# Kernel optimization log

Measured on AMD Instinct MI355X. Metric: run time of the kernel, lower is better.

Reference implementation:

```python
import jax, jax.numpy as jnp
import numpy as np

N, E, D_IN, L, H, U = 20000, 320000, 256, 4, 4, 64
HID = H * U  # 256
OUT = 64
LN_EPS = 1e-3  # keras LayerNormalization default epsilon
NEG_SLOPE = 0.2


def layer_norm(x, g, b):
    m = jnp.mean(x, axis=-1, keepdims=True)
    v = jnp.var(x, axis=-1, keepdims=True)
    return (x - m) * jax.lax.rsqrt(v + LN_EPS) * g + b


def gatv2(x, dst, src, Wl, Wr, a):
    # x: [N, HID]; Wl/Wr: [HID, H, U]; a: [H, U]
    zl = jnp.einsum('nd,dhu->nhu', x, Wl)  # target projection
    zr = jnp.einsum('nd,dhu->nhu', x, Wr)  # source projection / messages
    f = jax.nn.leaky_relu(zl[dst] + zr[src], NEG_SLOPE)       # [E, H, U]
    s = jnp.einsum('ehu,hu->eh', f, a)                        # [E, H]
    smax = jax.ops.segment_max(s, dst, num_segments=N)        # [N, H]
    es = jnp.exp(s - smax[dst])
    denom = jax.ops.segment_sum(es, dst, num_segments=N)      # [N, H]
    agg = jax.ops.segment_sum(es[:, :, None] * zr[src], dst, num_segments=N)
    agg = agg / (denom[:, :, None] + 1e-9)                    # [N, H, U]
    return agg.reshape(N, HID) + x  # residual (input dim == H*U)


def setup_inputs() -> dict:
    key = jax.random.key(0)
    ks = jax.random.split(key, 10)
    s_in = 1.0 / np.sqrt(D_IN)
    s_h = 1.0 / np.sqrt(HID)
    return {
        'x': jax.random.normal(ks[0], (N, D_IN), jnp.float32),
        'head_W': jax.random.normal(ks[1], (D_IN, HID), jnp.float32) * s_in,
        'head_b': jnp.zeros((HID,), jnp.float32),
        'ng_g': jnp.ones((L, HID), jnp.float32),
        'ng_b': jnp.zeros((L, HID), jnp.float32),
        'Wl': jax.random.normal(ks[2], (L, HID, H, U), jnp.float32) * s_h,
        'Wr': jax.random.normal(ks[3], (L, HID, H, U), jnp.float32) * s_h,
        'att': jax.random.normal(ks[4], (L, H, U), jnp.float32) * (1.0 / np.sqrt(U)),
        'nd_g': jnp.ones((L, HID), jnp.float32),
        'nd_b': jnp.zeros((L, HID), jnp.float32),
        'dense_W': jax.random.normal(ks[5], (L, HID, 4 * HID), jnp.float32) * s_h,
        'dense_b': jnp.zeros((L, 4 * HID), jnp.float32),
        'tail_W': jax.random.normal(ks[6], (HID, OUT), jnp.float32) * s_h,
        'tail_b': jnp.zeros((OUT,), jnp.float32),
        'edges': jax.random.randint(ks[7], (E, 2), 0, N, jnp.int32),
    }


def reference(x, head_W, head_b, ng_g, ng_b, Wl, Wr, att, nd_g, nd_b,
              dense_W, dense_b, tail_W, tail_b, edges):
    dst, src = edges[:, 0], edges[:, 1]
    h = x @ head_W + head_b  # head_layer
    for l in range(L):
        h = layer_norm(h, ng_g[l], ng_b[l])
        h = gatv2(h, dst, src, Wl[l], Wr[l], att[l])
        xr = layer_norm(h, nd_g[l], nd_b[l])
        # inference: dropout is identity
        d = jax.nn.gelu(xr @ dense_W[l] + dense_b[l], approximate=True)  # [N, 4*HID]
        h = d.reshape(N, 4, HID).sum(axis=1) + xr  # Add(split(.,4)) + residual
    return h @ tail_W + tail_b
```

## Files before the change

### kernel.cpp

```cpp
#include <hip/hip_runtime.h>
#include <cstdint>

#define NN 20000
#define EE 320000
#define DHID 256

typedef short bf16x8 __attribute__((ext_vector_type(8)));
typedef float f32x4 __attribute__((ext_vector_type(4)));


__device__ __forceinline__ float b2f(unsigned short u) {
    union { unsigned int i; float f; } v;
    v.i = ((unsigned int)u) << 16;
    return v.f;
}

__device__ __forceinline__ void b2f2(unsigned int w, float& lo, float& hi) {
    union { unsigned int i; float f; } a, c;
    a.i = w << 16;
    c.i = w & 0xffff0000u;
    lo = a.f;
    hi = c.f;
}

__device__ __forceinline__ unsigned short f2b(float x) {
    union { float f; unsigned int i; } v;
    v.f = x;
    unsigned int r = (v.i + 0x7FFFu + ((v.i >> 16) & 1u)) >> 16;
    return (unsigned short)r;
}

__device__ __forceinline__ float wave_sum(float v) {
#pragma unroll
    for (int m = 1; m < 64; m <<= 1) v += __shfl_xor(v, m);
    return v;
}

__device__ __forceinline__ float quad16_sum(float v) {
#pragma unroll
    for (int m = 1; m < 16; m <<= 1) v += __shfl_xor(v, m);
    return v;
}

__device__ __forceinline__ float gelu_f(float x) {
    float z = 0.7978845608028654f * (x + 0.044715f * x * x * x);
    float e = __expf(2.0f * z);
    float t = 1.0f - 2.0f / (e + 1.0f);
    return 0.5f * x * (1.0f + t);
}

__device__ __forceinline__ void gld16(const unsigned short* g, unsigned short* lds) {
    __builtin_amdgcn_global_load_lds((const __attribute__((address_space(1))) unsigned int*)g,
                                     (__attribute__((address_space(3))) unsigned int*)lds, 16, 0, 0);
}


__global__ void hist_kernel(const int* __restrict__ edges, int* __restrict__ counts, int E_) {
    int e = blockIdx.x * 256 + threadIdx.x;
    if (e >= E_) return;
    atomicAdd(&counts[edges[e * 2]], 1);
}

__global__ __launch_bounds__(1024) void scan_block(const int* __restrict__ counts,
                                                   int* __restrict__ excl,
                                                   int* __restrict__ bsums, int n) {
    __shared__ int sd[1024];
    int tid = threadIdx.x;
    int i = blockIdx.x * 1024 + tid;
    int c = (i < n) ? counts[i] : 0;
    sd[tid] = c;
    __syncthreads();
#pragma unroll
    for (int off = 1; off < 1024; off <<= 1) {
        int v = (tid >= off) ? sd[tid - off] : 0;
        __syncthreads();
        sd[tid] += v;
        __syncthreads();
    }
    if (i < n) excl[i] = sd[tid] - c;
    if (tid == 1023) bsums[blockIdx.x] = sd[1023];
}

__global__ void scan_tops(int* __restrict__ bsums, int nb) {
    if (threadIdx.x == 0 && blockIdx.x == 0) {
        int run = 0;
        for (int i = 0; i < nb; ++i) { int t = bsums[i]; bsums[i] = run; run += t; }
    }
}

__global__ void scan_fix(const int* __restrict__ excl, const int* __restrict__ bsums,
                         int* __restrict__ indptr, int* __restrict__ cursor, int n) {
    int i = blockIdx.x * 256 + threadIdx.x;
    if (i < n) {
        int v = excl[i] + bsums[i >> 10];
        indptr[i] = v;
        cursor[i] = v;
    }
    if (i == 0) indptr[n] = EE;
}

__global__ void scatter_kernel(const int* __restrict__ edges, int* __restrict__ cursor,
                               int* __restrict__ ssrc, int E_) {
    int e = blockIdx.x * 256 + threadIdx.x;
    if (e >= E_) return;
    int dstn = edges[e * 2];
    int src  = edges[e * 2 + 1];
    int pos = atomicAdd(&cursor[dstn], 1);
    ssrc[pos] = src;
}


__global__ __launch_bounds__(256) void transpose_bf16(const float* __restrict__ W,
                                                      unsigned short* __restrict__ Wt,
                                                      int K, int M, size_t lsW, size_t lsT) {
    W  += (size_t)blockIdx.z * lsW;
    Wt += (size_t)blockIdx.z * lsT;
    __shared__ float sm[32][33];
    int m0 = blockIdx.x * 32, k0 = blockIdx.y * 32;
    int tx = threadIdx.x & 31, ty = threadIdx.x >> 5;
#pragma unroll
    for (int i = 0; i < 4; ++i)
        sm[ty + i * 8][tx] = W[(size_t)(k0 + ty + i * 8) * M + m0 + tx];
    __syncthreads();
#pragma unroll
    for (int i = 0; i < 4; ++i)
        Wt[(size_t)(m0 + ty + i * 8) * K + k0 + tx] = f2b(sm[tx][ty + i * 8]);
}

__global__ void convert_bf16(const float* __restrict__ in, unsigned short* __restrict__ out, int n4) {
    int i = blockIdx.x * 256 + threadIdx.x;
    if (i >= n4) return;
    float4 v = *(const float4*)(in + (size_t)i * 4);
    ushort4 o;
    o.x = f2b(v.x); o.y = f2b(v.y); o.z = f2b(v.z); o.w = f2b(v.w);
    *(ushort4*)(out + (size_t)i * 4) = o;
}


__global__ __launch_bounds__(256) void ln_kernel(const float* __restrict__ X,
                                                 const float* __restrict__ g,
                                                 const float* __restrict__ b,
                                                 float* __restrict__ Y,
                                                 unsigned short* __restrict__ Yb, int nrows) {
    int row = blockIdx.x * 4 + (threadIdx.x >> 6);
    int lane = threadIdx.x & 63;
    if (row >= nrows) return;
    float4 v = *(const float4*)(X + (size_t)row * DHID + lane * 4);
    float sum = wave_sum(v.x + v.y + v.z + v.w);
    float sq  = wave_sum(v.x * v.x + v.y * v.y + v.z * v.z + v.w * v.w);
    float mean = sum * (1.0f / DHID);
    float var  = sq * (1.0f / DHID) - mean * mean;
    float r = rsqrtf(fmaxf(var, 0.0f) + 1e-3f);
    float4 gv = *(const float4*)(g + lane * 4);
    float4 bv = *(const float4*)(b + lane * 4);
    float4 o;
    o.x = (v.x - mean) * r * gv.x + bv.x;
    o.y = (v.y - mean) * r * gv.y + bv.y;
    o.z = (v.z - mean) * r * gv.z + bv.z;
    o.w = (v.w - mean) * r * gv.w + bv.w;
    *(float4*)(Y + (size_t)row * DHID + lane * 4) = o;
    ushort4 ob;
    ob.x = f2b(o.x); ob.y = f2b(o.y); ob.z = f2b(o.z); ob.w = f2b(o.w);
    *(ushort4*)(Yb + (size_t)row * DHID + lane * 4) = ob;
}

__global__ __launch_bounds__(256) void ln_dense(const unsigned short* __restrict__ d,
                                                const float* __restrict__ xr,
                                                const float* __restrict__ g,
                                                const float* __restrict__ b,
                                                float* __restrict__ Y,
                                                unsigned short* __restrict__ Yb, int nrows) {
    int row = blockIdx.x * 4 + (threadIdx.x >> 6);
    int lane = threadIdx.x & 63;
    if (row >= nrows) return;
    float4 v = *(const float4*)(xr + (size_t)row * DHID + lane * 4);
#pragma unroll
    for (int c = 0; c < 4; ++c) {
        ushort4 t = *(const ushort4*)(d + (size_t)row * 1024 + c * 256 + lane * 4);
        v.x += b2f(t.x); v.y += b2f(t.y); v.z += b2f(t.z); v.w += b2f(t.w);
    }
    float sum = wave_sum(v.x + v.y + v.z + v.w);
    float sq  = wave_sum(v.x * v.x + v.y * v.y + v.z * v.z + v.w * v.w);
    float mean = sum * (1.0f / DHID);
    float var  = sq * (1.0f / DHID) - mean * mean;
    float r = rsqrtf(fmaxf(var, 0.0f) + 1e-3f);
    float4 gv = *(const float4*)(g + lane * 4);
    float4 bv = *(const float4*)(b + lane * 4);
    float4 o;
    o.x = (v.x - mean) * r * gv.x + bv.x;
    o.y = (v.y - mean) * r * gv.y + bv.y;
    o.z = (v.z - mean) * r * gv.z + bv.z;
    o.w = (v.w - mean) * r * gv.w + bv.w;
    *(float4*)(Y + (size_t)row * DHID + lane * 4) = o;
    ushort4 ob;
    ob.x = f2b(o.x); ob.y = f2b(o.y); ob.z = f2b(o.z); ob.w = f2b(o.w);
    *(ushort4*)(Yb + (size_t)row * DHID + lane * 4) = ob;
}

__global__ __launch_bounds__(256) void combine_final(const unsigned short* __restrict__ d,
                                                     const float* __restrict__ xr,
                                                     unsigned short* __restrict__ hb, int nrows) {
    int row = blockIdx.x * 4 + (threadIdx.x >> 6);
    int lane = threadIdx.x & 63;
    if (row >= nrows) return;
    float4 v = *(const float4*)(xr + (size_t)row * DHID + lane * 4);
#pragma unroll
    for (int c = 0; c < 4; ++c) {
        ushort4 t = *(const ushort4*)(d + (size_t)row * 1024 + c * 256 + lane * 4);
        v.x += b2f(t.x); v.y += b2f(t.y); v.z += b2f(t.z); v.w += b2f(t.w);
    }
    ushort4 ob;
    ob.x = f2b(v.x); ob.y = f2b(v.y); ob.z = f2b(v.z); ob.w = f2b(v.w);
    *(ushort4*)(hb + (size_t)row * DHID + lane * 4) = ob;
}


#define CS_STRIDE 140

template <int EP>
__global__ __launch_bounds__(256, 3) void gemm128(const unsigned short* __restrict__ A,
                                                  const unsigned short* __restrict__ B,
                                                  const float* __restrict__ bias,
                                                  void* __restrict__ Cv, int nrows, int ncols) {
    __shared__ unsigned short As[128 * 32];
    __shared__ unsigned short Bs[128 * 32];
    __shared__ unsigned short Cs[128 * CS_STRIDE];
    const int bm = blockIdx.x * 128, bn = blockIdx.y * 128;
    if (bm >= nrows) return;
    const int tid  = threadIdx.x;
    const int w    = tid >> 6, lane = tid & 63;
    const int quad = lane >> 4, l16 = lane & 15;
    const int wm = w >> 1, wn = w & 1;

    const int srow = lane & 15;
    const int sg   = lane >> 4;
    int ga0 = min(bm + w * 32 + srow,      nrows - 1);
    int ga1 = min(bm + w * 32 + 16 + srow, nrows - 1);
    int gb0 = min(bn + w * 32 + srow,      ncols - 1);
    int gb1 = min(bn + w * 32 + 16 + srow, ncols - 1);
    const unsigned short* Ap0 = A + (size_t)ga0 * 256 + sg * 8;
    const unsigned short* Ap1 = A + (size_t)ga1 * 256 + sg * 8;
    const unsigned short* Bp0 = B + (size_t)gb0 * 256 + sg * 8;
    const unsigned short* Bp1 = B + (size_t)gb1 * 256 + sg * 8;
    unsigned short* la0 = As + (2 * w) * 512;
    unsigned short* la1 = As + (2 * w + 1) * 512;
    unsigned short* lb0 = Bs + (2 * w) * 512;
    unsigned short* lb1 = Bs + (2 * w + 1) * 512;

    f32x4 acc[4][4] = {};
    for (int k0 = 0; k0 < 256; k0 += 32) {
        gld16(Ap0 + k0, la0);
        gld16(Ap1 + k0, la1);
        gld16(Bp0 + k0, lb0);
        gld16(Bp1 + k0, lb1);
        __syncthreads();
        bf16x8 a[4], b[4];
#pragma unroll
        for (int mi = 0; mi < 4; ++mi)
            a[mi] = *(const bf16x8*)(As + (wm * 4 + mi) * 512 + quad * 128 + l16 * 8);
#pragma unroll
        for (int ni = 0; ni < 4; ++ni)
            b[ni] = *(const bf16x8*)(Bs + (wn * 4 + ni) * 512 + quad * 128 + l16 * 8);
#pragma unroll
        for (int mi = 0; mi < 4; ++mi)
#pragma unroll
            for (int ni = 0; ni < 4; ++ni)
                acc[mi][ni] = __builtin_amdgcn_mfma_f32_16x16x32_bf16(a[mi], b[ni], acc[mi][ni], 0, 0, 0);
        __syncthreads();
    }

    if (EP == 0) {
#pragma unroll
        for (int ni = 0; ni < 4; ++ni) {
            int col = bn + wn * 64 + ni * 16 + l16;
            if (col >= ncols) continue;
            float bv = bias ? bias[col] : 0.0f;
#pragma unroll
            for (int mi = 0; mi < 4; ++mi) {
#pragma unroll
                for (int r = 0; r < 4; ++r) {
                    int row = bm + wm * 64 + mi * 16 + quad * 4 + r;
                    if (row < nrows) ((float*)Cv)[(size_t)row * ncols + col] = acc[mi][ni][r] + bv;
                }
            }
        }
    } else {
#pragma unroll
        for (int ni = 0; ni < 4; ++ni) {
            int lc = wn * 64 + ni * 16 + l16;
            float bv = (EP == 2) ? bias[bn + lc] : 0.0f;
#pragma unroll
            for (int mi = 0; mi < 4; ++mi) {
#pragma unroll
                for (int r = 0; r < 4; ++r) {
                    int lr = wm * 64 + mi * 16 + quad * 4 + r;
                    float v = acc[mi][ni][r] + bv;
                    Cs[lr * CS_STRIDE + lc] = f2b(EP == 2 ? gelu_f(v) : v);
                }
            }
        }
        __syncthreads();
#pragma unroll
        for (int i = 0; i < 8; ++i) {
            int id = tid + 256 * i;
            int lr = id >> 4;
            int lc = (id & 15) * 8;
            int grow = bm + lr;
            if (grow < nrows) {
                uint4 val = *(const uint4*)(Cs + lr * CS_STRIDE + lc);
                *(uint4*)((unsigned short*)Cv + (size_t)grow * ncols + bn + lc) = val;
            }
        }
    }
}


__global__ __launch_bounds__(256) void gat_fused(const unsigned short* __restrict__ zb,
                                                 const float* __restrict__ att,
                                                 const int* __restrict__ ssrc,
                                                 const int* __restrict__ indptr,
                                                 const float* __restrict__ hn,
                                                 const float* __restrict__ g,
                                                 const float* __restrict__ b,
                                                 float* __restrict__ xr,
                                                 unsigned short* __restrict__ xrb, int nrows) {
    int wid = threadIdx.x >> 6;
    int lane = threadIdx.x & 63;
    int n = blockIdx.x * 4 + wid;
    if (n >= nrows) return;
    int start = indptr[n];
    int end = indptr[n + 1];

    ushort4 zlu = *(const ushort4*)(zb + (size_t)n * 512 + lane * 4);
    float zl0 = b2f(zlu.x), zl1 = b2f(zlu.y), zl2 = b2f(zlu.z), zl3 = b2f(zlu.w);
    float4 a4 = *(const float4*)(att + lane * 4);
    size_t idx = (size_t)n * DHID + lane * 4;
    float4 rres = *(const float4*)(hn + idx);

    float m = -3.0e38f, denom = 0.f;
    float ax = 0.f, ay = 0.f, az = 0.f, aw = 0.f;

    const uint2* zrp = (const uint2*)(zb + 256);
    uint2 c0 = make_uint2(0, 0), c1 = make_uint2(0, 0);
    if (start < end) {
        int i0 = ssrc[start];
        int i1 = ssrc[(start + 1 < end) ? start + 1 : start];
        c0 = zrp[(size_t)i0 * 128 + lane];
        c1 = zrp[(size_t)i1 * 128 + lane];
    }
    for (int p = start; p < end; p += 2) {
        uint2 u0 = c0, u1 = c1;
        bool val1 = (p + 1 < end);
        if (p + 2 < end) {
            int j0 = ssrc[p + 2];
            int j1 = ssrc[(p + 3 < end) ? p + 3 : p + 2];
            c0 = zrp[(size_t)j0 * 128 + lane];
            c1 = zrp[(size_t)j1 * 128 + lane];
        }
        float z00, z01, z02, z03, z10, z11, z12, z13;
        b2f2(u0.x, z00, z01); b2f2(u0.y, z02, z03);
        b2f2(u1.x, z10, z11); b2f2(u1.y, z12, z13);

        float v0 = zl0 + z00, v1 = zl1 + z01, v2 = zl2 + z02, v3 = zl3 + z03;
        float t0 = zl0 + z10, t1 = zl1 + z11, t2 = zl2 + z12, t3 = zl3 + z13;
        v0 = (v0 > 0.f) ? v0 : 0.2f * v0;
        v1 = (v1 > 0.f) ? v1 : 0.2f * v1;
        v2 = (v2 > 0.f) ? v2 : 0.2f * v2;
        v3 = (v3 > 0.f) ? v3 : 0.2f * v3;
        t0 = (t0 > 0.f) ? t0 : 0.2f * t0;
        t1 = (t1 > 0.f) ? t1 : 0.2f * t1;
        t2 = (t2 > 0.f) ? t2 : 0.2f * t2;
        t3 = (t3 > 0.f) ? t3 : 0.2f * t3;
        float part0 = a4.x * v0 + a4.y * v1 + a4.z * v2 + a4.w * v3;
        float part1 = a4.x * t0 + a4.y * t1 + a4.z * t2 + a4.w * t3;
        float sp0 = quad16_sum(part0);
        float sp1 = quad16_sum(part1);
        if (!val1) sp1 = -3.0e38f;
        float newm = fmaxf(m, fmaxf(sp0, sp1));
        float corr = __expf(m - newm);
        float w0 = __expf(sp0 - newm);
        float w1 = __expf(sp1 - newm);
        denom = denom * corr + w0 + w1;
        ax = ax * corr + w0 * z00 + w1 * z10;
        ay = ay * corr + w0 * z01 + w1 * z11;
        az = az * corr + w0 * z02 + w1 * z12;
        aw = aw * corr + w0 * z03 + w1 * z13;
        m = newm;
    }
    float inv = 1.0f / (denom + 1e-9f);
    float4 o;
    o.x = ax * inv + rres.x;
    o.y = ay * inv + rres.y;
    o.z = az * inv + rres.z;
    o.w = aw * inv + rres.w;
    float sum = wave_sum(o.x + o.y + o.z + o.w);
    float sq  = wave_sum(o.x * o.x + o.y * o.y + o.z * o.z + o.w * o.w);
    float mean = sum * (1.0f / DHID);
    float var  = sq * (1.0f / DHID) - mean * mean;
    float rr = rsqrtf(fmaxf(var, 0.0f) + 1e-3f);
    float4 gv = *(const float4*)(g + lane * 4);
    float4 bv = *(const float4*)(b + lane * 4);
    float4 y;
    y.x = (o.x - mean) * rr * gv.x + bv.x;
    y.y = (o.y - mean) * rr * gv.y + bv.y;
    y.z = (o.z - mean) * rr * gv.z + bv.z;
    y.w = (o.w - mean) * rr * gv.w + bv.w;
    *(float4*)(xr + idx) = y;
    ushort4 ob;
    ob.x = f2b(y.x); ob.y = f2b(y.y); ob.z = f2b(y.z); ob.w = f2b(y.w);
    *(ushort4*)(xrb + idx) = ob;
}


extern "C" void kernel_launch(void* const* d_in, const int* in_sizes, int n_in,
                              void* d_out, int out_size, void* d_ws, size_t ws_size,
                              hipStream_t stream) {
    const float* x       = (const float*)d_in[0];
    const float* head_W  = (const float*)d_in[1];
    const float* head_b  = (const float*)d_in[2];
    const float* ng_g    = (const float*)d_in[3];
    const float* ng_b    = (const float*)d_in[4];
    const float* Wl      = (const float*)d_in[5];
    const float* Wr      = (const float*)d_in[6];
    const float* att     = (const float*)d_in[7];
    const float* nd_g    = (const float*)d_in[8];
    const float* nd_b    = (const float*)d_in[9];
    const float* dense_W = (const float*)d_in[10];
    const float* dense_b = (const float*)d_in[11];
    const float* tail_W  = (const float*)d_in[12];
    const float* tail_b  = (const float*)d_in[13];
    const int*   edges   = (const int*)d_in[14];
    float* out = (float*)d_out;

    const size_t NH = (size_t)NN * DHID;
    float* xr = (float*)d_ws;
    float* hn = xr + NH;
    unsigned short* hnb = (unsigned short*)(hn + NH);
    unsigned short* xrb = hnb + NH;
    unsigned short* U   = xrb + NH;
    unsigned short* zb  = U;
    unsigned short* d_buf = U;
    unsigned short* headT  = U + 4 * NH;
    unsigned short* WzT    = headT + 65536;
    unsigned short* denseT = WzT + 524288;
    unsigned short* tailT  = denseT + 1048576;
    int* counts = (int*)(tailT + 16384);
    int* bsums  = counts + NN;
    int* excl   = bsums + 32;
    int* indptr = excl + NN;
    int* cursor = indptr + NN + 1;
    int* ssrc   = cursor + NN;

    hipMemsetAsync(counts, 0, NN * sizeof(int), stream);
    hist_kernel<<<(EE + 255) / 256, 256, 0, stream>>>(edges, counts, EE);
    scan_block<<<(NN + 1023) / 1024, 1024, 0, stream>>>(counts, excl, bsums, NN);
    scan_tops<<<1, 64, 0, stream>>>(bsums, (NN + 1023) / 1024);
    scan_fix<<<(NN + 255) / 256, 256, 0, stream>>>(excl, bsums, indptr, cursor, NN);
    scatter_kernel<<<(EE + 255) / 256, 256, 0, stream>>>(edges, cursor, ssrc, EE);

    transpose_bf16<<<dim3(8, 8, 1), 256, 0, stream>>>(head_W, headT, 256, 256, 0, 0);
    transpose_bf16<<<dim3(8, 8, 4), 256, 0, stream>>>(Wl, WzT, 256, 256, 65536, 131072);
    transpose_bf16<<<dim3(8, 8, 4), 256, 0, stream>>>(Wr, WzT + 65536, 256, 256, 65536, 131072);
    transpose_bf16<<<dim3(32, 8, 4), 256, 0, stream>>>(dense_W, denseT, 256, 1024, 262144, 262144);
    transpose_bf16<<<dim3(2, 8, 1), 256, 0, stream>>>(tail_W, tailT, 256, 64, 0, 0);
    convert_bf16<<<(int)(NH / 4 + 255) / 256, 256, 0, stream>>>(x, hnb, (int)(NH / 4));

    const int GXP = 160;
    gemm128<0><<<dim3(GXP, 2), 256, 0, stream>>>(hnb, headT, head_b, xr, NN, 256);

    for (int l = 0; l < 4; ++l) {
        if (l == 0)
            ln_kernel<<<NN / 4, 256, 0, stream>>>(xr, ng_g, ng_b, hn, hnb, NN);
        else
            ln_dense<<<NN / 4, 256, 0, stream>>>(d_buf, xr, ng_g + l * 256, ng_b + l * 256, hn, hnb, NN);
        gemm128<1><<<dim3(GXP, 4), 256, 0, stream>>>(hnb, WzT + (size_t)l * 131072, nullptr, zb, NN, 512);
        gat_fused<<<(NN + 3) / 4, 256, 0, stream>>>(zb, att + l * 256, ssrc, indptr, hn,
                                                    nd_g + l * 256, nd_b + l * 256, xr, xrb, NN);
        gemm128<2><<<dim3(GXP, 8), 256, 0, stream>>>(xrb, denseT + (size_t)l * 262144,
                                                     dense_b + l * 1024, d_buf, NN, 1024);
    }
    combine_final<<<NN / 4, 256, 0, stream>>>(d_buf, xr, hnb, NN);
    gemm128<0><<<dim3(GXP, 1), 256, 0, stream>>>(hnb, tailT, tail_b, out, NN, 64);
}
```

Measured before the change: 644.8 us.

## Alias GEMM epilogue staging onto tile smem and unroll GAT edge loop by four

```diff
diff --git a/kernel.cpp b/kernel.cpp
--- a/kernel.cpp
+++ b/kernel.cpp
@@ -215,16 +215,17 @@
 }
 
 
-#define CS_STRIDE 140
+#define CS 132
 
 template <int EP>
-__global__ __launch_bounds__(256, 3) void gemm128(const unsigned short* __restrict__ A,
+__global__ __launch_bounds__(256, 5) void gemm128(const unsigned short* __restrict__ A,
                                                   const unsigned short* __restrict__ B,
                                                   const float* __restrict__ bias,
                                                   void* __restrict__ Cv, int nrows, int ncols) {
-    __shared__ unsigned short As[128 * 32];
-    __shared__ unsigned short Bs[128 * 32];
-    __shared__ unsigned short Cs[128 * CS_STRIDE];
+    __shared__ unsigned short smem[8448];
+    unsigned short* As = smem;
+    unsigned short* Bs = smem + 4096;
+    unsigned short* Cs = smem;
     const int bm = blockIdx.x * 128, bn = blockIdx.y * 128;
     if (bm >= nrows) return;
     const int tid  = threadIdx.x;
@@ -286,30 +287,36 @@
         }
     } else {
 #pragma unroll
-        for (int ni = 0; ni < 4; ++ni) {
-            int lc = wn * 64 + ni * 16 + l16;
-            float bv = (EP == 2) ? bias[bn + lc] : 0.0f;
-#pragma unroll
-            for (int mi = 0; mi < 4; ++mi) {
-#pragma unroll
-                for (int r = 0; r < 4; ++r) {
-                    int lr = wm * 64 + mi * 16 + quad * 4 + r;
-                    float v = acc[mi][ni][r] + bv;
-                    Cs[lr * CS_STRIDE + lc] = f2b(EP == 2 ? gelu_f(v) : v);
+        for (int half = 0; half < 2; ++half) {
+            if (wm == half) {
+#pragma unroll
+                for (int ni = 0; ni < 4; ++ni) {
+                    int lc = wn * 64 + ni * 16 + l16;
+                    float bv = (EP == 2) ? bias[bn + lc] : 0.0f;
+#pragma unroll
+                    for (int mi = 0; mi < 4; ++mi) {
+#pragma unroll
+                        for (int r = 0; r < 4; ++r) {
+                            int lr = mi * 16 + quad * 4 + r;
+                            float v = acc[mi][ni][r] + bv;
+                            Cs[lr * CS + lc] = f2b(EP == 2 ? gelu_f(v) : v);
+                        }
+                    }
                 }
             }
-        }
-        __syncthreads();
-#pragma unroll
-        for (int i = 0; i < 8; ++i) {
-            int id = tid + 256 * i;
-            int lr = id >> 4;
-            int lc = (id & 15) * 8;
-            int grow = bm + lr;
-            if (grow < nrows) {
-                uint4 val = *(const uint4*)(Cs + lr * CS_STRIDE + lc);
-                *(uint4*)((unsigned short*)Cv + (size_t)grow * ncols + bn + lc) = val;
+            __syncthreads();
+#pragma unroll
+            for (int i = 0; i < 4; ++i) {
+                int id = tid + 256 * i;
+                int lr = id >> 4;
+                int lc = (id & 15) * 8;
+                int grow = bm + half * 64 + lr;
+                if (grow < nrows) {
+                    uint4 val = *(const uint4*)(Cs + lr * CS + lc);
+                    *(uint4*)((unsigned short*)Cv + (size_t)grow * ncols + bn + lc) = val;
+                }
             }
+            __syncthreads();
         }
     }
 }
@@ -341,50 +348,55 @@
     float ax = 0.f, ay = 0.f, az = 0.f, aw = 0.f;
 
     const uint2* zrp = (const uint2*)(zb + 256);
-    uint2 c0 = make_uint2(0, 0), c1 = make_uint2(0, 0);
+    uint2 c[4];
+#pragma unroll
+    for (int j = 0; j < 4; ++j) c[j] = make_uint2(0, 0);
     if (start < end) {
-        int i0 = ssrc[start];
-        int i1 = ssrc[(start + 1 < end) ? start + 1 : start];
-        c0 = zrp[(size_t)i0 * 128 + lane];
-        c1 = zrp[(size_t)i1 * 128 + lane];
-    }
-    for (int p = start; p < end; p += 2) {
-        uint2 u0 = c0, u1 = c1;
-        bool val1 = (p + 1 < end);
-        if (p + 2 < end) {
-            int j0 = ssrc[p + 2];
-            int j1 = ssrc[(p + 3 < end) ? p + 3 : p + 2];
-            c0 = zrp[(size_t)j0 * 128 + lane];
-            c1 = zrp[(size_t)j1 * 128 + lane];
+#pragma unroll
+        for (int j = 0; j < 4; ++j) {
+            int q = min(start + j, end - 1);
+            c[j] = zrp[(size_t)ssrc[q] * 128 + lane];
         }
-        float z00, z01, z02, z03, z10, z11, z12, z13;
-        b2f2(u0.x, z00, z01); b2f2(u0.y, z02, z03);
-        b2f2(u1.x, z10, z11); b2f2(u1.y, z12, z13);
-
-        float v0 = zl0 + z00, v1 = zl1 + z01, v2 = zl2 + z02, v3 = zl3 + z03;
-        float t0 = zl0 + z10, t1 = zl1 + z11, t2 = zl2 + z12, t3 = zl3 + z13;
-        v0 = (v0 > 0.f) ? v0 : 0.2f * v0;
-        v1 = (v1 > 0.f) ? v1 : 0.2f * v1;
-        v2 = (v2 > 0.f) ? v2 : 0.2f * v2;
-        v3 = (v3 > 0.f) ? v3 : 0.2f * v3;
-        t0 = (t0 > 0.f) ? t0 : 0.2f * t0;
-        t1 = (t1 > 0.f) ? t1 : 0.2f * t1;
-        t2 = (t2 > 0.f) ? t2 : 0.2f * t2;
-        t3 = (t3 > 0.f) ? t3 : 0.2f * t3;
-        float part0 = a4.x * v0 + a4.y * v1 + a4.z * v2 + a4.w * v3;
-        float part1 = a4.x * t0 + a4.y * t1 + a4.z * t2 + a4.w * t3;
-        float sp0 = quad16_sum(part0);
-        float sp1 = quad16_sum(part1);
-        if (!val1) sp1 = -3.0e38f;
-        float newm = fmaxf(m, fmaxf(sp0, sp1));
+    }
+    for (int p = start; p < end; p += 4) {
+        uint2 u[4];
+#pragma unroll
+        for (int j = 0; j < 4; ++j) u[j] = c[j];
+        if (p + 4 < end) {
+#pragma unroll
+            for (int j = 0; j < 4; ++j) {
+                int q = min(p + 4 + j, end - 1);
+                c[j] = zrp[(size_t)ssrc[q] * 128 + lane];
+            }
+        }
+        float z[4][4], sp[4];
+#pragma unroll
+        for (int j = 0; j < 4; ++j) {
+            b2f2(u[j].x, z[j][0], z[j][1]);
+            b2f2(u[j].y, z[j][2], z[j][3]);
+            float v0 = zl0 + z[j][0], v1 = zl1 + z[j][1];
+            float v2 = zl2 + z[j][2], v3 = zl3 + z[j][3];
+            v0 = (v0 > 0.f) ? v0 : 0.2f * v0;
+            v1 = (v1 > 0.f) ? v1 : 0.2f * v1;
+            v2 = (v2 > 0.f) ? v2 : 0.2f * v2;
+            v3 = (v3 > 0.f) ? v3 : 0.2f * v3;
+            float part = a4.x * v0 + a4.y * v1 + a4.z * v2 + a4.w * v3;
+            sp[j] = quad16_sum(part);
+        }
+#pragma unroll
+        for (int j = 1; j < 4; ++j)
+            if (p + j >= end) sp[j] = -3.0e38f;
+        float newm = fmaxf(fmaxf(m, fmaxf(sp[0], sp[1])), fmaxf(sp[2], sp[3]));
         float corr = __expf(m - newm);
-        float w0 = __expf(sp0 - newm);
-        float w1 = __expf(sp1 - newm);
-        denom = denom * corr + w0 + w1;
-        ax = ax * corr + w0 * z00 + w1 * z10;
-        ay = ay * corr + w0 * z01 + w1 * z11;
-        az = az * corr + w0 * z02 + w1 * z12;
-        aw = aw * corr + w0 * z03 + w1 * z13;
+        float w0 = __expf(sp[0] - newm);
+        float w1 = __expf(sp[1] - newm);
+        float w2 = __expf(sp[2] - newm);
+        float w3 = __expf(sp[3] - newm);
+        denom = denom * corr + w0 + w1 + w2 + w3;
+        ax = ax * corr + w0 * z[0][0] + w1 * z[1][0] + w2 * z[2][0] + w3 * z[3][0];
+        ay = ay * corr + w0 * z[0][1] + w1 * z[1][1] + w2 * z[2][1] + w3 * z[3][1];
+        az = az * corr + w0 * z[0][2] + w1 * z[1][2] + w2 * z[2][2] + w3 * z[3][2];
+        aw = aw * corr + w0 * z[0][3] + w1 * z[1][3] + w2 * z[2][3] + w3 * z[3][3];
         m = newm;
     }
     float inv = 1.0f / (denom + 1e-9f);
```

Result: slower. 670.5 us (+4.0%).
